# Performance work log

Hardware: AMD Instinct MI355X
Metric: run time of the kernel (lower is better)

The kernel has to match this reference:

```python
import jax, jax.numpy as jnp
import numpy as np

B, N, D = 16, 10000, 128
EPS = 1e-5


def setup_inputs() -> dict:
    key = jax.random.key(0)
    ks = jax.random.split(key, 8)
    h = jax.random.normal(ks[0], (B, N, D), dtype=jnp.float32)
    # tour must be a permutation per batch row (scatter assumes bijectivity)
    tour = jax.vmap(lambda k: jax.random.permutation(k, N))(jax.random.split(ks[1], B)).astype(jnp.int64)
    s = 0.02
    return {
        "h": h,
        "tour": tour,
        "W1m": jax.random.normal(ks[2], (2 * D, D), dtype=jnp.float32) * s,
        "b1m": jnp.zeros((D,), jnp.float32),
        "W2m": jax.random.normal(ks[3], (D, D), dtype=jnp.float32) * s,
        "b2m": jnp.zeros((D,), jnp.float32),
        "W1u": jax.random.normal(ks[4], (2 * D, D), dtype=jnp.float32) * s,
        "b1u": jnp.zeros((D,), jnp.float32),
        "W2u": jax.random.normal(ks[5], (D, D), dtype=jnp.float32) * s,
        "b2u": jnp.zeros((D,), jnp.float32),
        "gamma": jnp.ones((D,), jnp.float32),
        "beta": jnp.zeros((D,), jnp.float32),
    }


def _mlp(x, W1, b1, W2, b2):
    # Linear -> SiLU -> Linear
    y = jax.nn.silu(jnp.einsum("bne,ed->bnd", x, W1) + b1)
    return jnp.einsum("bnd,de->bne", y, W2) + b2


def _layernorm(x, gamma, beta):
    mu = jnp.mean(x, axis=-1, keepdims=True)
    var = jnp.var(x, axis=-1, keepdims=True)
    return (x - mu) * jax.lax.rsqrt(var + EPS) * gamma + beta


def reference(h, tour, W1m, b1m, W2m, b2m, W1u, b1u, W2u, b2u, gamma, beta):
    # gather node features in tour order: h_pos[b, i] = h[b, tour[b, i]]
    h_pos = jnp.take_along_axis(h, tour[..., None], axis=1)  # (B, N, D)
    h_prev = jnp.roll(h_pos, 1, axis=1)
    h_next = jnp.roll(h_pos, -1, axis=1)
    msg = (_mlp(jnp.concatenate([h_pos, h_prev], axis=-1), W1m, b1m, W2m, b2m)
           + _mlp(jnp.concatenate([h_pos, h_next], axis=-1), W1m, b1m, W2m, b2m))
    h_new_pos = _mlp(jnp.concatenate([h_pos, msg], axis=-1), W1u, b1u, W2u, b2u)
    h_new_pos = _layernorm(h_pos + h_new_pos, gamma, beta)
    # scatter back to original node order (tour is a permutation)
    bidx = jnp.arange(h.shape[0])[:, None]
    h_new = jnp.zeros_like(h).at[bidx, tour].set(h_new_pos)
    return h_new
```

## Files before the change

### kernel.cpp

```cpp
#include <hip/hip_runtime.h>


#define BB 16
#define NN 10000
#define DD 128
#define TT 62
#define NTHREADS 256
#define EPS_LN 1e-5f

typedef __attribute__((ext_vector_type(8))) short short8v;
typedef __attribute__((ext_vector_type(8))) unsigned short ushort8v;
typedef __attribute__((ext_vector_type(4))) float f32x4;

__device__ __forceinline__ unsigned short bf16_rne(float f) {
    union { float f; unsigned u; } v; v.f = f;
    unsigned r = v.u + 0x7FFFu + ((v.u >> 16) & 1u);
    return (unsigned short)(r >> 16);
}
__device__ __forceinline__ float bf16f(unsigned short h) {
    union { unsigned u; float f; } v; v.u = ((unsigned)h) << 16;
    return v.f;
}
__device__ __forceinline__ float silu_f(float x) { return x / (1.0f + __expf(-x)); }

__device__ __forceinline__ int tour_at(const int* tw, bool is64, long long i) {
    int v = is64 ? (int)(((const long long*)tw)[i]) : tw[i];
    return (v < 0 || v >= NN) ? 0 : v;
}

__device__ __forceinline__ int swz(int row, int k) {
    return (((k >> 3) ^ (row & 7)) << 4) | ((k & 7) << 1);
}

__global__ void pack_weights(const float* __restrict__ W1m, const float* __restrict__ W2m,
                             const float* __restrict__ W1u, const float* __restrict__ W2u,
                             unsigned short* __restrict__ wp)
{
    int t = blockIdx.x * blockDim.x + threadIdx.x;
    if (t >= 6 * 128 * 16) return;
    int img = t >> 11;
    int r   = t & 2047;
    int n   = r >> 4;
    int g   = r & 15;
    const float* src; int koff;
    switch (img) {
      case 0: src = W1m; koff = 128; break;
      case 1: src = W1m; koff = 0;   break;
      case 2: src = W2m; koff = 0;   break;
      case 3: src = W1u; koff = 0;   break;
      case 4: src = W1u; koff = 128; break;
      default: src = W2u; koff = 0;  break;
    }
    ushort8v v;
    #pragma unroll
    for (int j = 0; j < 8; ++j) {
        int k = g * 8 + j;
        v[j] = bf16_rne(src[(koff + k) * 128 + n]);
    }
    *(ushort8v*)((char*)wp + img * 32768 + n * 256 + ((g ^ (n & 7)) << 4)) = v;
}

__global__ __launch_bounds__(NTHREADS, 2)
void gnn_mfma_kernel(const float* __restrict__ h, const int* __restrict__ tour_raw,
                     const unsigned short* __restrict__ wp,
                     const float* __restrict__ b1m, const float* __restrict__ b2m,
                     const float* __restrict__ b1u, const float* __restrict__ b2u,
                     const float* __restrict__ gma, const float* __restrict__ bta,
                     float* __restrict__ out)
{
    __shared__ unsigned char lds[81920];
    unsigned char* XA = lds;
    unsigned char* CB = lds + 16384;
    unsigned char* SB = lds + 32768;
    unsigned char* WS = lds + 49152;

    const int tid  = threadIdx.x;
    const int b    = blockIdx.y;
    const int t0   = blockIdx.x * TT;
    const int Tl   = min(TT, NN - t0);
    const int lane = tid & 63;
    const int w    = tid >> 6;
    const int dl   = lane & 15;

    const bool is64 = (tour_raw[1] == 0) && (tour_raw[3] == 0);
    const long long tbase = (long long)b * NN;
    const float* hb = h + (long long)b * NN * DD;

    float vb1m[8], vb2m[8], vb1u[8], vb2u[8], vg[8], vbt[8];
    #pragma unroll
    for (int nt = 0; nt < 8; ++nt) {
        int d = nt * 16 + dl;
        vb1m[nt] = b1m[d]; vb2m[nt] = b2m[d];
        vb1u[nt] = b1u[d]; vb2u[nt] = b2u[d];
        vg[nt]   = gma[d]; vbt[nt]  = bta[d];
    }

    #pragma unroll
    for (int p = 0; p < 4; ++p) {
        int id  = tid + p * NTHREADS;
        int row = id >> 4;
        int gg  = id & 15;
        int gi;
        if (row < TT)       gi = (row < Tl) ? (t0 + row) : t0;
        else if (row == TT) gi = (t0 == 0) ? (NN - 1) : (t0 - 1);
        else                gi = (t0 + Tl >= NN) ? 0 : (t0 + Tl);
        int node = tour_at(tour_raw, is64, tbase + gi);
        const float4 f0 = *(const float4*)(hb + node * DD + gg * 8);
        const float4 f1 = *(const float4*)(hb + node * DD + gg * 8 + 4);
        ushort8v vv;
        vv[0] = bf16_rne(f0.x); vv[1] = bf16_rne(f0.y); vv[2] = bf16_rne(f0.z); vv[3] = bf16_rne(f0.w);
        vv[4] = bf16_rne(f1.x); vv[5] = bf16_rne(f1.y); vv[6] = bf16_rne(f1.z); vv[7] = bf16_rne(f1.w);
        *(ushort8v*)(XA + row * 256 + ((gg ^ (row & 7)) << 4)) = vv;
    }

    f32x4 acc[8], acc_a[8], acc_z[8];
    short8v afr[4];
    ushort8v wreg[8];

    auto wload = [&](int img) {
        #pragma unroll
        for (int r = 0; r < 8; ++r)
            wreg[r] = *(const ushort8v*)((const char*)wp + img * 32768 + r * 4096 + tid * 16);
    };
    auto wstore = [&]() {
        #pragma unroll
        for (int r = 0; r < 8; ++r)
            *(ushort8v*)(WS + r * 4096 + tid * 16) = wreg[r];
    };
    auto load_afrag = [&](const unsigned char* P) {
        int row = w * 16 + (lane & 15);
        #pragma unroll
        for (int ks = 0; ks < 4; ++ks) {
            int g = ks * 4 + (lane >> 4);
            afr[ks] = *(const short8v*)(P + row * 256 + ((g ^ (row & 7)) << 4));
        }
    };
    auto zero8 = [&](f32x4* A) {
        #pragma unroll
        for (int nt = 0; nt < 8; ++nt) A[nt] = (f32x4){0.f, 0.f, 0.f, 0.f};
    };
    auto gemm_acc = [&](f32x4* A) {
        #pragma unroll
        for (int ks = 0; ks < 4; ++ks) {
            #pragma unroll
            for (int nt = 0; nt < 8; ++nt) {
                int n = nt * 16 + dl;
                int g = ks * 4 + (lane >> 4);
                short8v bf = *(const short8v*)(WS + n * 256 + ((g ^ (n & 7)) << 4));
                A[nt] = __builtin_amdgcn_mfma_f32_16x16x32_bf16(afr[ks], bf, A[nt], 0, 0, 0);
            }
        }
    };
    auto store_cd = [&](unsigned char* P, f32x4* A) {
        #pragma unroll
        for (int nt = 0; nt < 8; ++nt) {
            int d = nt * 16 + dl;
            #pragma unroll
            for (int reg = 0; reg < 4; ++reg) {
                int row = w * 16 + (lane >> 4) * 4 + reg;
                *(unsigned short*)(P + row * 256 + swz(row, d)) = bf16_rne(A[nt][reg]);
            }
        }
    };

    wload(0);

    __syncthreads();
    wstore(); wload(1);
    load_afrag(XA);
    zero8(acc);
    __syncthreads();
    gemm_acc(acc);
    store_cd(CB, acc);

    __syncthreads();
    wstore(); wload(2);
    zero8(acc_a);
    __syncthreads();
    gemm_acc(acc_a);
    #pragma unroll
    for (int nt = 0; nt < 8; ++nt) {
        int d = nt * 16 + dl;
        #pragma unroll
        for (int reg = 0; reg < 4; ++reg) {
            int row = w * 16 + (lane >> 4) * 4 + reg;
            int jp = (row == 0) ? 62 : row - 1;
            int jn = (row >= Tl - 1) ? 63 : row + 1;
            float aij = acc_a[nt][reg] + vb1m[nt];
            float cp = bf16f(*(const unsigned short*)(CB + jp * 256 + swz(jp, d)));
            float cn = bf16f(*(const unsigned short*)(CB + jn * 256 + swz(jn, d)));
            acc_a[nt][reg] = silu_f(aij + cp) + silu_f(aij + cn);
        }
    }
    store_cd(SB, acc_a);

    __syncthreads();
    wstore(); wload(3);
    load_afrag(SB);
    zero8(acc);
    __syncthreads();
    gemm_acc(acc);
    #pragma unroll
    for (int nt = 0; nt < 8; ++nt) {
        #pragma unroll
        for (int reg = 0; reg < 4; ++reg) acc[nt][reg] += 2.0f * vb2m[nt];
    }
    store_cd(SB, acc);

    __syncthreads();
    wstore(); wload(4);
    load_afrag(XA);
    zero8(acc_z);
    __syncthreads();
    gemm_acc(acc_z);

    __syncthreads();
    wstore(); wload(5);
    load_afrag(SB);
    __syncthreads();
    gemm_acc(acc_z);
    #pragma unroll
    for (int nt = 0; nt < 8; ++nt) {
        #pragma unroll
        for (int reg = 0; reg < 4; ++reg)
            acc_z[nt][reg] = silu_f(acc_z[nt][reg] + vb1u[nt]);
    }
    store_cd(SB, acc_z);

    __syncthreads();
    wstore();
    load_afrag(SB);
    zero8(acc);
    __syncthreads();
    gemm_acc(acc);

    #pragma unroll
    for (int reg = 0; reg < 4; ++reg) {
        int row = w * 16 + (lane >> 4) * 4 + reg;
        bool valid = row < Tl;
        int node = tour_at(tour_raw, is64, tbase + t0 + (valid ? row : 0));
        float r8[8]; float s1 = 0.f, s2 = 0.f;
        #pragma unroll
        for (int nt = 0; nt < 8; ++nt) {
            int d = nt * 16 + dl;
            float xg = hb[node * DD + d];
            float rv = xg + acc[nt][reg] + vb2u[nt];
            r8[nt] = rv; s1 += rv; s2 += rv * rv;
        }
        #pragma unroll
        for (int m = 1; m <= 8; m <<= 1) {
            s1 += __shfl_xor(s1, m, 64);
            s2 += __shfl_xor(s2, m, 64);
        }
        float mu  = s1 * (1.0f / 128.0f);
        float var = s2 * (1.0f / 128.0f) - mu * mu;
        float rs  = rsqrtf(var + EPS_LN);
        if (valid) {
            float* op = out + ((long long)b * NN + node) * DD;
            #pragma unroll
            for (int nt = 0; nt < 8; ++nt) {
                int d = nt * 16 + dl;
                op[d] = (r8[nt] - mu) * rs * vg[nt] + vbt[nt];
            }
        }
    }
}

extern "C" void kernel_launch(void* const* d_in, const int* in_sizes, int n_in,
                              void* d_out, int out_size, void* d_ws, size_t ws_size,
                              hipStream_t stream)
{
    const float* h    = (const float*)d_in[0];
    const int*   tour = (const int*)d_in[1];
    const float* W1m  = (const float*)d_in[2];
    const float* b1m  = (const float*)d_in[3];
    const float* W2m  = (const float*)d_in[4];
    const float* b2m  = (const float*)d_in[5];
    const float* W1u  = (const float*)d_in[6];
    const float* b1u  = (const float*)d_in[7];
    const float* W2u  = (const float*)d_in[8];
    const float* b2u  = (const float*)d_in[9];
    const float* gma  = (const float*)d_in[10];
    const float* bta  = (const float*)d_in[11];
    float*       out  = (float*)d_out;
    unsigned short* wp = (unsigned short*)d_ws;

    pack_weights<<<48, NTHREADS, 0, stream>>>(W1m, W2m, W1u, W2u, wp);

    dim3 grid((NN + TT - 1) / TT, BB);
    gnn_mfma_kernel<<<grid, NTHREADS, 0, stream>>>(h, tour, wp, b1m, b2m, b1u, b2u,
                                                   gma, bta, out);
}
```

Baseline: 256.0 us.

## Stage final GEMM output through LDS for vectorized LayerNorm epilogue and coalesced stores

```diff
diff --git a/kernel.cpp b/kernel.cpp
--- a/kernel.cpp
+++ b/kernel.cpp
@@ -1,4 +1,5 @@
 #include <hip/hip_runtime.h>
+#include <hip/hip_bf16.h>
 
 
 #define BB 16
@@ -9,13 +10,15 @@
 #define EPS_LN 1e-5f
 
 typedef __attribute__((ext_vector_type(8))) short short8v;
-typedef __attribute__((ext_vector_type(8))) unsigned short ushort8v;
 typedef __attribute__((ext_vector_type(4))) float f32x4;
 
-__device__ __forceinline__ unsigned short bf16_rne(float f) {
-    union { float f; unsigned u; } v; v.f = f;
-    unsigned r = v.u + 0x7FFFu + ((v.u >> 16) & 1u);
-    return (unsigned short)(r >> 16);
+__device__ __forceinline__ unsigned short cvt_bf16(float f) {
+    __hip_bfloat16 h = __float2bfloat16(f);
+    union { __hip_bfloat16 h; unsigned short u; } cv; cv.h = h; return cv.u;
+}
+__device__ __forceinline__ unsigned cvt2_bf16(float a, float b) {
+    __hip_bfloat162 h2 = __float22bfloat162_rn(make_float2(a, b));
+    union { __hip_bfloat162 h; unsigned u; } cv; cv.h = h2; return cv.u;
 }
 __device__ __forceinline__ float bf16f(unsigned short h) {
     union { unsigned u; float f; } v; v.u = ((unsigned)h) << 16;
@@ -37,11 +40,10 @@
                              unsigned short* __restrict__ wp)
 {
     int t = blockIdx.x * blockDim.x + threadIdx.x;
-    if (t >= 6 * 128 * 16) return;
-    int img = t >> 11;
-    int r   = t & 2047;
-    int n   = r >> 4;
-    int g   = r & 15;
+    int img = t >> 12;
+    int r   = t & 4095;
+    int k   = r >> 5;
+    int n4  = (r & 31) * 4;
     const float* src; int koff;
     switch (img) {
       case 0: src = W1m; koff = 128; break;
@@ -51,13 +53,15 @@
       case 4: src = W1u; koff = 128; break;
       default: src = W2u; koff = 0;  break;
     }
-    ushort8v v;
-    #pragma unroll
-    for (int j = 0; j < 8; ++j) {
-        int k = g * 8 + j;
-        v[j] = bf16_rne(src[(koff + k) * 128 + n]);
-    }
-    *(ushort8v*)((char*)wp + img * 32768 + n * 256 + ((g ^ (n & 7)) << 4)) = v;
+    const float4 v = *(const float4*)(src + (koff + k) * 128 + n4);
+    const float vs[4] = {v.x, v.y, v.z, v.w};
+    const int g = k >> 3, klo = (k & 7) * 2;
+    #pragma unroll
+    for (int i = 0; i < 4; ++i) {
+        int n = n4 + i;
+        *(unsigned short*)((char*)wp + img * 32768 + n * 256 + ((g ^ (n & 7)) << 4) + klo)
+            = cvt_bf16(vs[i]);
+    }
 }
 
 __global__ __launch_bounds__(NTHREADS, 2)
@@ -73,6 +77,7 @@
     unsigned char* CB = lds + 16384;
     unsigned char* SB = lds + 32768;
     unsigned char* WS = lds + 49152;
+    float* VS = (float*)(lds + 16384);
 
     const int tid  = threadIdx.x;
     const int b    = blockIdx.y;
@@ -81,19 +86,26 @@
     const int lane = tid & 63;
     const int w    = tid >> 6;
     const int dl   = lane & 15;
+    const int lg   = lane >> 4;
 
     const bool is64 = (tour_raw[1] == 0) && (tour_raw[3] == 0);
     const long long tbase = (long long)b * NN;
     const float* hb = h + (long long)b * NN * DD;
 
-    float vb1m[8], vb2m[8], vb1u[8], vb2u[8], vg[8], vbt[8];
+    float vb1m[8], vb2m_2[8], vb1u[8];
     #pragma unroll
     for (int nt = 0; nt < 8; ++nt) {
         int d = nt * 16 + dl;
-        vb1m[nt] = b1m[d]; vb2m[nt] = b2m[d];
-        vb1u[nt] = b1u[d]; vb2u[nt] = b2u[d];
-        vg[nt]   = gma[d]; vbt[nt]  = bta[d];
-    }
+        vb1m[nt] = b1m[d]; vb2m_2[nt] = 2.0f * b2m[d]; vb1u[nt] = b1u[d];
+    }
+
+    int ofsB[4], ofsA[4];
+    #pragma unroll
+    for (int ks = 0; ks < 4; ++ks) {
+        ofsB[ks] = dl * 256 + (((ks * 4 + lg) ^ (dl & 7)) << 4);
+        ofsA[ks] = ofsB[ks] + w * 4096;
+    }
+    const unsigned char* pB[4] = {WS + ofsB[0], WS + ofsB[1], WS + ofsB[2], WS + ofsB[3]};
 
     #pragma unroll
     for (int p = 0; p < 4; ++p) {
@@ -107,33 +119,30 @@
         int node = tour_at(tour_raw, is64, tbase + gi);
         const float4 f0 = *(const float4*)(hb + node * DD + gg * 8);
         const float4 f1 = *(const float4*)(hb + node * DD + gg * 8 + 4);
-        ushort8v vv;
-        vv[0] = bf16_rne(f0.x); vv[1] = bf16_rne(f0.y); vv[2] = bf16_rne(f0.z); vv[3] = bf16_rne(f0.w);
-        vv[4] = bf16_rne(f1.x); vv[5] = bf16_rne(f1.y); vv[6] = bf16_rne(f1.z); vv[7] = bf16_rne(f1.w);
-        *(ushort8v*)(XA + row * 256 + ((gg ^ (row & 7)) << 4)) = vv;
+        uint4 vv;
+        vv.x = cvt2_bf16(f0.x, f0.y); vv.y = cvt2_bf16(f0.z, f0.w);
+        vv.z = cvt2_bf16(f1.x, f1.y); vv.w = cvt2_bf16(f1.z, f1.w);
+        *(uint4*)(XA + row * 256 + ((gg ^ (row & 7)) << 4)) = vv;
     }
 
     f32x4 acc[8], acc_a[8], acc_z[8];
     short8v afr[4];
-    ushort8v wreg[8];
-
-    auto wload = [&](int img) {
+    uint4 wfull[8];
+
+    auto wload8 = [&](int img) {
         #pragma unroll
         for (int r = 0; r < 8; ++r)
-            wreg[r] = *(const ushort8v*)((const char*)wp + img * 32768 + r * 4096 + tid * 16);
-    };
-    auto wstore = [&]() {
+            wfull[r] = *(const uint4*)((const char*)wp + img * 32768 + r * 4096 + tid * 16);
+    };
+    auto wstore8 = [&]() {
         #pragma unroll
         for (int r = 0; r < 8; ++r)
-            *(ushort8v*)(WS + r * 4096 + tid * 16) = wreg[r];
-    };
-    auto load_afrag = [&](const unsigned char* P) {
-        int row = w * 16 + (lane & 15);
-        #pragma unroll
-        for (int ks = 0; ks < 4; ++ks) {
-            int g = ks * 4 + (lane >> 4);
-            afr[ks] = *(const short8v*)(P + row * 256 + ((g ^ (row & 7)) << 4));
-        }
+            *(uint4*)(WS + r * 4096 + tid * 16) = wfull[r];
+    };
+    auto load_afrag = [&](int pofs) {
+        #pragma unroll
+        for (int ks = 0; ks < 4; ++ks)
+            afr[ks] = *(const short8v*)(lds + pofs + ofsA[ks]);
     };
     auto zero8 = [&](f32x4* A) {
         #pragma unroll
@@ -144,37 +153,36 @@
         for (int ks = 0; ks < 4; ++ks) {
             #pragma unroll
             for (int nt = 0; nt < 8; ++nt) {
-                int n = nt * 16 + dl;
-                int g = ks * 4 + (lane >> 4);
-                short8v bf = *(const short8v*)(WS + n * 256 + ((g ^ (n & 7)) << 4));
+                short8v bf = *(const short8v*)(pB[ks] + nt * 4096);
                 A[nt] = __builtin_amdgcn_mfma_f32_16x16x32_bf16(afr[ks], bf, A[nt], 0, 0, 0);
             }
         }
     };
     auto store_cd = [&](unsigned char* P, f32x4* A) {
         #pragma unroll
-        for (int nt = 0; nt < 8; ++nt) {
-            int d = nt * 16 + dl;
+        for (int reg = 0; reg < 4; ++reg) {
+            int row = w * 16 + lg * 4 + reg;
+            int b0  = ((dl >> 3) ^ row) & 1;
+            int crs = (((row & 7) >> 1)) << 5;
+            unsigned char* base = P + row * 256 + (b0 << 4) + ((dl & 7) << 1);
             #pragma unroll
-            for (int reg = 0; reg < 4; ++reg) {
-                int row = w * 16 + (lane >> 4) * 4 + reg;
-                *(unsigned short*)(P + row * 256 + swz(row, d)) = bf16_rne(A[nt][reg]);
-            }
-        }
-    };
-
-    wload(0);
-
-    __syncthreads();
-    wstore(); wload(1);
-    load_afrag(XA);
+            for (int nt = 0; nt < 8; ++nt)
+                *(unsigned short*)(base + ((nt << 5) ^ crs)) = cvt_bf16(A[nt][reg]);
+        }
+    };
+
+    wload8(0);
+
+    __syncthreads();
+    wstore8(); wload8(1);
+    load_afrag(0);
     zero8(acc);
     __syncthreads();
     gemm_acc(acc);
     store_cd(CB, acc);
 
     __syncthreads();
-    wstore(); wload(2);
+    wstore8(); wload8(2);
     zero8(acc_a);
     __syncthreads();
     gemm_acc(acc_a);
@@ -183,7 +191,7 @@
         int d = nt * 16 + dl;
         #pragma unroll
         for (int reg = 0; reg < 4; ++reg) {
-            int row = w * 16 + (lane >> 4) * 4 + reg;
+            int row = w * 16 + lg * 4 + reg;
             int jp = (row == 0) ? 62 : row - 1;
             int jn = (row >= Tl - 1) ? 63 : row + 1;
             float aij = acc_a[nt][reg] + vb1m[nt];
@@ -195,72 +203,93 @@
     store_cd(SB, acc_a);
 
     __syncthreads();
-    wstore(); wload(3);
-    load_afrag(SB);
+    wstore8(); wload8(3);
+    load_afrag(32768);
     zero8(acc);
     __syncthreads();
     gemm_acc(acc);
     #pragma unroll
-    for (int nt = 0; nt < 8; ++nt) {
-        #pragma unroll
-        for (int reg = 0; reg < 4; ++reg) acc[nt][reg] += 2.0f * vb2m[nt];
-    }
+    for (int nt = 0; nt < 8; ++nt)
+        #pragma unroll
+        for (int reg = 0; reg < 4; ++reg) acc[nt][reg] += vb2m_2[nt];
     store_cd(SB, acc);
 
     __syncthreads();
-    wstore(); wload(4);
-    load_afrag(XA);
+    wstore8(); wload8(4);
+    load_afrag(0);
     zero8(acc_z);
     __syncthreads();
     gemm_acc(acc_z);
 
     __syncthreads();
-    wstore(); wload(5);
-    load_afrag(SB);
+    wstore8(); wload8(5);
+    load_afrag(32768);
     __syncthreads();
     gemm_acc(acc_z);
     #pragma unroll
-    for (int nt = 0; nt < 8; ++nt) {
+    for (int nt = 0; nt < 8; ++nt)
         #pragma unroll
         for (int reg = 0; reg < 4; ++reg)
             acc_z[nt][reg] = silu_f(acc_z[nt][reg] + vb1u[nt]);
-    }
     store_cd(SB, acc_z);
 
     __syncthreads();
-    wstore();
-    load_afrag(SB);
+    wstore8();
+    load_afrag(32768);
     zero8(acc);
     __syncthreads();
     gemm_acc(acc);
 
     #pragma unroll
-    for (int reg = 0; reg < 4; ++reg) {
-        int row = w * 16 + (lane >> 4) * 4 + reg;
-        bool valid = row < Tl;
-        int node = tour_at(tour_raw, is64, tbase + t0 + (valid ? row : 0));
-        float r8[8]; float s1 = 0.f, s2 = 0.f;
-        #pragma unroll
-        for (int nt = 0; nt < 8; ++nt) {
-            int d = nt * 16 + dl;
-            float xg = hb[node * DD + d];
-            float rv = xg + acc[nt][reg] + vb2u[nt];
-            r8[nt] = rv; s1 += rv; s2 += rv * rv;
-        }
-        #pragma unroll
-        for (int m = 1; m <= 8; m <<= 1) {
-            s1 += __shfl_xor(s1, m, 64);
-            s2 += __shfl_xor(s2, m, 64);
-        }
-        float mu  = s1 * (1.0f / 128.0f);
-        float var = s2 * (1.0f / 128.0f) - mu * mu;
-        float rs  = rsqrtf(var + EPS_LN);
+    for (int nt = 0; nt < 8; ++nt) {
+        #pragma unroll
+        for (int reg = 0; reg < 4; ++reg) {
+            int row = w * 16 + lg * 4 + reg;
+            VS[row * 128 + ((nt ^ (row & 7)) << 4) + dl] = acc[nt][reg];
+        }
+    }
+    __syncthreads();
+
+    {
+        const int row = tid >> 2;
+        const int d0  = (tid & 3) * 32;
+        const bool valid = row < Tl;
+        const int node = tour_at(tour_raw, is64, tbase + t0 + (valid ? row : 0));
+        const float* xg = hb + node * DD + d0;
+        const int r7 = row & 7;
+        f32x4 r[8];
+        float s1 = 0.f, s2 = 0.f;
+        #pragma unroll
+        for (int c = 0; c < 8; ++c) {
+            const int d = d0 + c * 4;
+            const f32x4 v = *(const f32x4*)&VS[row * 128 + (((d >> 4) ^ r7) << 4) + (d & 15)];
+            const float4 x = *(const float4*)(xg + c * 4);
+            const float4 bb = *(const float4*)(b2u + d);
+            r[c][0] = x.x + v[0] + bb.x;
+            r[c][1] = x.y + v[1] + bb.y;
+            r[c][2] = x.z + v[2] + bb.z;
+            r[c][3] = x.w + v[3] + bb.w;
+            #pragma unroll
+            for (int j = 0; j < 4; ++j) { s1 += r[c][j]; s2 += r[c][j] * r[c][j]; }
+        }
+        s1 += __shfl_xor(s1, 1, 64); s2 += __shfl_xor(s2, 1, 64);
+        s1 += __shfl_xor(s1, 2, 64); s2 += __shfl_xor(s2, 2, 64);
+        const float mu  = s1 * (1.0f / 128.0f);
+        const float var = s2 * (1.0f / 128.0f) - mu * mu;
+        const float rs  = rsqrtf(var + EPS_LN);
         if (valid) {
-            float* op = out + ((long long)b * NN + node) * DD;
+            float* op = out + ((long long)b * NN + node) * DD + d0;
             #pragma unroll
-            for (int nt = 0; nt < 8; ++nt) {
-                int d = nt * 16 + dl;
-                op[d] = (r8[nt] - mu) * rs * vg[nt] + vbt[nt];
+            for (int c = 0; c < 8; ++c) {
+                const int d = d0 + c * 4;
+                const float4 g4 = *(const float4*)(gma + d);
+                const float4 t4 = *(const float4*)(bta + d);
+                float4 o;
+                o.x = (r[c][0] - mu) * rs * g4.x + t4.x;
+                o.y = (r[c][1] - mu) * rs * g4.y + t4.y;
+                o.z = (r[c][2] - mu) * rs * g4.z + t4.z;
+                o.w = (r[c][3] - mu) * rs * g4.w + t4.w;
+                *(float4*)(op + c * 4) = o;
             }
         }
     }
@@ -285,7 +314,7 @@
     float*       out  = (float*)d_out;
     unsigned short* wp = (unsigned short*)d_ws;
 
-    pack_weights<<<48, NTHREADS, 0, stream>>>(W1m, W2m, W1u, W2u, wp);
+    pack_weights<<<96, NTHREADS, 0, stream>>>(W1m, W2m, W1u, W2u, wp);
 
     dim3 grid((NN + TT - 1) / TT, BB);
     gnn_mfma_kernel<<<grid, NTHREADS, 0, stream>>>(h, tour, wp, b1m, b2m, b1u, b2u,
```

New measurement: 377.8 us. 47.5% more time.
